# Performance work log

Measured on AMD Instinct MI355X. Metric: run time of the kernel, lower is better.

Reference implementation:

```python
import jax, jax.numpy as jnp
import numpy as np

TGT, BSZ, E, H, HD, P = 256, 64, 1024, 16, 64, 16
TAU = 3.0  # gumbel temperature
SCALE = 1.0 / np.sqrt(HD)


def setup_inputs() -> dict:
    rng = jax.random.key(0)
    ks = jax.random.split(rng, 14)
    n = lambda i, s: jax.random.normal(ks[i], s, dtype=jnp.float32)
    u = jax.random.uniform(ks[7], (BSZ, 2), dtype=jnp.float32, minval=1e-6, maxval=1.0 - 1e-6)
    return {
        'idx': 0,
        'query': n(0, (TGT, BSZ, E)),
        'key': n(1, (TGT, BSZ, E)),
        'value': n(2, (TGT, BSZ, E)),
        'prefix': n(3, (BSZ, 2, P, E)) * 0.5,  # gathered prefix_pool[prompt_ids]
        'batch_weight': jax.random.uniform(ks[4], (BSZ,), dtype=jnp.float32),
        'ori_image_features': n(5, (BSZ, 512)),
        'gumbel_noise': -jnp.log(-jnp.log(u)),  # standard gumbel(0,1) noise
        'in_proj_w': n(8, (3 * E, E)) * 0.02,
        'in_proj_b': jnp.zeros((3 * E,), jnp.float32),
        'out_w': n(9, (E, E)) * 0.02,
        'out_b': jnp.zeros((E,), jnp.float32),
        'gumbel_w': n(10, (2, 512)) * 0.05,
        'gumbel_b': jnp.zeros((2,), jnp.float32),
    }


def _sdpa(q, k, v):
    # q:[b,h,t,d] k,v:[b,h,s,d]
    s = jnp.einsum('bhtd,bhsd->bhts', q, k) * SCALE
    a = jax.nn.softmax(s, axis=-1)
    return jnp.einsum('bhts,bhsd->bhtd', a, v)


def reference(idx, query, key, value, prefix, batch_weight, ori_image_features,
              gumbel_noise, in_proj_w, in_proj_b, out_w, out_b, gumbel_w, gumbel_b):
    tgt, bsz, e = query.shape
    src = key.shape[0]
    # packed in-projection (w chunked into q/k/v blocks)
    w_q, w_k, w_v = jnp.split(in_proj_w, 3, axis=0)
    b_q, b_k, b_v = jnp.split(in_proj_b, 3, axis=0)
    q = query @ w_q.T + b_q            # [t,b,E]
    k = key @ w_k.T + b_k              # [s,b,E]
    v = value @ w_v.T + b_v
    # -> [b,h,t,d]
    q = q.reshape(tgt, bsz, H, HD).transpose(1, 2, 0, 3)
    k = k.reshape(src, bsz, H, HD).transpose(1, 2, 0, 3)
    v = v.reshape(src, bsz, H, HD).transpose(1, 2, 0, 3)
    # prefix k/v: [b,P,E] -> [b,h,P,d] (no in-projection, used raw as in source)
    pk = prefix[:, 0].reshape(bsz, P, H, HD).transpose(0, 2, 1, 3)
    pv = prefix[:, 1].reshape(bsz, P, H, HD).transpose(0, 2, 1, 3)

    attn = _sdpa(q, k, v)                      # [b,h,t,d]
    attn_flat = attn.transpose(2, 0, 1, 3).reshape(tgt * bsz, e)  # (t,b) row order

    attn_pre = _sdpa(q, pk, pv) * batch_weight[:, None, None, None]
    attn_pre_flat = attn_pre.transpose(2, 0, 1, 3).reshape(tgt * bsz, e)

    # gumbel-softmax gate (soft), one 2-way gate per sample
    logits = ori_image_features @ gumbel_w.T + gumbel_b           # [b,2]
    gumbel = jax.nn.softmax((logits + gumbel_noise) / TAU, axis=-1)
    gate = jnp.repeat(gumbel, tgt, axis=0)                        # [b*t,2] (b,t) order, as in source
    combined = attn_flat * gate[:, :1] + (attn_flat + attn_pre_flat) * gate[:, 1:2]

    out = combined @ out_w.T + out_b
    return out.reshape(tgt, bsz, e)
```

## Files before the change

kernel.cpp:

```cpp
#include <hip/hip_runtime.h>

typedef __attribute__((ext_vector_type(8))) short bf16x8;
typedef __attribute__((ext_vector_type(4))) float f32x4;
typedef __attribute__((ext_vector_type(8))) unsigned short ushort8;
typedef __attribute__((ext_vector_type(4))) unsigned short ushort4v;
typedef __attribute__((ext_vector_type(4))) float float4v;
typedef __attribute__((ext_vector_type(2))) unsigned int uint2v;
typedef __attribute__((ext_vector_type(4))) unsigned int uint4v;

#define TGT 256
#define BSZ 64
#define EMB 1024
#define NH 16
#define HD 64
#define PP 16

__device__ __forceinline__ float b2f(unsigned short u) {
  return __builtin_bit_cast(float, ((unsigned int)u) << 16);
}
__device__ __forceinline__ unsigned short f2b(float f) {
  unsigned int u = __builtin_bit_cast(unsigned int, f);
  u += 0x7fffu + ((u >> 16) & 1u);
  return (unsigned short)(u >> 16);
}
__device__ __forceinline__ unsigned int pack2(float lo, float hi) {
  return (unsigned int)f2b(lo) | ((unsigned int)f2b(hi) << 16);
}
__device__ __forceinline__ f32x4 mfma16(bf16x8 a, bf16x8 b, f32x4 c) {
  return __builtin_amdgcn_mfma_f32_16x16x32_bf16(a, b, c, 0, 0, 0);
}
__device__ __forceinline__ void gl_lds16(const unsigned short* g, unsigned short* l) {
  __builtin_amdgcn_global_load_lds(
      (const __attribute__((address_space(1))) unsigned int*)g,
      (__attribute__((address_space(3))) unsigned int*)l, 16, 0, 0);
}

__global__ __launch_bounds__(64) void gate_kernel(
    const float* __restrict__ feat, const float* __restrict__ gw,
    const float* __restrict__ gb, const float* __restrict__ noise,
    float* __restrict__ g1) {
  const int b = blockIdx.x, lane = threadIdx.x;
  float a0 = 0.f, a1 = 0.f;
  for (int i = lane; i < 512; i += 64) {
    float f = feat[b * 512 + i];
    a0 += f * gw[i];
    a1 += f * gw[512 + i];
  }
#pragma unroll
  for (int off = 32; off >= 1; off >>= 1) {
    a0 += __shfl_xor(a0, off);
    a1 += __shfl_xor(a1, off);
  }
  if (lane == 0) {
    float l0 = (a0 + gb[0] + noise[b * 2 + 0]) * (1.0f / 3.0f);
    float l1 = (a1 + gb[1] + noise[b * 2 + 1]) * (1.0f / 3.0f);
    float mm = fmaxf(l0, l1);
    float e0 = __expf(l0 - mm), e1 = __expf(l1 - mm);
    g1[b] = e1 / (e0 + e1);
  }
}

__global__ __launch_bounds__(256) void cast_bf16_kernel(
    const float* __restrict__ in, unsigned short* __restrict__ out, int n8) {
  int i = blockIdx.x * blockDim.x + threadIdx.x;
  const int stride = gridDim.x * blockDim.x;
  for (; i < n8; i += stride) {
    const float4v* p = (const float4v*)(in + (size_t)i * 8);
    float4v v0 = p[0], v1 = p[1];
    ushort8 o = {f2b(v0[0]), f2b(v0[1]), f2b(v0[2]), f2b(v0[3]),
                 f2b(v1[0]), f2b(v1[1]), f2b(v1[2]), f2b(v1[3])};
    *(ushort8*)(out + (size_t)i * 8) = o;
  }
}

#define A128_ISSUE(t)                                    \
  {                                                      \
    const float* _p = a32p + (size_t)(t) * 32;           \
    ar[(t) & 1][0] = *(const float4v*)_p;                \
    ar[(t) & 1][1] = *(const float4v*)(_p + 4);          \
  }
#define A128_WRITE(t)                                                   \
  {                                                                     \
    float4v* v = ar[(t) & 1];                                           \
    uint4v h = {pack2(v[0][0], v[0][1]), pack2(v[0][2], v[0][3]),       \
                pack2(v[1][0], v[1][1]), pack2(v[1][2], v[1][3])};      \
    *(uint4v*)&As[(t) & 1][swA] = h;                                    \
  }
#define B128_STAGE(s)                                    \
  {                                                      \
    int k0s = (s) * 32;                                  \
    unsigned short* d = &Bs[(s) & 3][wl];                \
    gl_lds16(b0p + k0s, d);                              \
    gl_lds16(b1p + k0s, d + 4096);                       \
  }
#define G128_STEP(s, DO_IA, DO_SB, DO_W)                              \
  {                                                                   \
    const unsigned short* Ab = &As[(s) & 1][0];                       \
    const unsigned short* Bb = &Bs[(s) & 3][0];                       \
    bf16x8 af[4], bfr[4];                                             \
    _Pragma("unroll") for (int mi = 0; mi < 4; ++mi)                  \
        af[mi] = *(const bf16x8*)&Ab[aoff + mi * 512];                \
    _Pragma("unroll") for (int ni = 0; ni < 2; ++ni)                  \
        bfr[ni] = *(const bf16x8*)&Bb[boff + ni * 512];               \
    if (DO_IA) A128_ISSUE((s) + 2);                                   \
    __builtin_amdgcn_s_barrier();                                     \
    __builtin_amdgcn_s_setprio(1);                                    \
    _Pragma("unroll") for (int mi = 0; mi < 4; ++mi) {                \
      acc[mi][0] = mfma16(af[mi], bfr[0], acc[mi][0]);                \
      acc[mi][1] = mfma16(af[mi], bfr[1], acc[mi][1]);                \
    }                                                                 \
    __builtin_amdgcn_s_setprio(0);                                    \
    __builtin_amdgcn_s_barrier();                                     \
    _Pragma("unroll") for (int ni = 2; ni < 4; ++ni)                  \
        bfr[ni] = *(const bf16x8*)&Bb[boff + ni * 512];               \
    if (DO_SB) B128_STAGE((s) + 3);                                   \
    __builtin_amdgcn_s_barrier();                                     \
    __builtin_amdgcn_s_setprio(1);                                    \
    _Pragma("unroll") for (int mi = 0; mi < 4; ++mi) {                \
      acc[mi][2] = mfma16(af[mi], bfr[2], acc[mi][2]);                \
      acc[mi][3] = mfma16(af[mi], bfr[3], acc[mi][3]);                \
    }                                                                 \
    __builtin_amdgcn_s_setprio(0);                                    \
    if (DO_W) A128_WRITE((s) + 1);                                    \
  }
#define STEP_WAIT(cntstr)                                \
  asm volatile("s_waitcnt " cntstr ::: "memory");        \
  __builtin_amdgcn_sched_barrier(0);                     \
  __builtin_amdgcn_s_barrier();

template <int QSCALE>
__global__ __launch_bounds__(512, 4) void gemm128f_kernel(
    const float* __restrict__ A, const unsigned short* __restrict__ W,
    const float* __restrict__ bias, unsigned short* __restrict__ Cv) {
  constexpr int K = 1024, N = 1024;
  __shared__ __attribute__((aligned(16))) unsigned short As[2][4096];
  __shared__ __attribute__((aligned(16))) unsigned short Bs[4][8192];
  const int tid = threadIdx.x;
  const int wv = tid >> 6, lane = tid & 63;
  const int l15 = lane & 15, kg = lane >> 4;
  const int bid = blockIdx.x;
  const int cpx = gridDim.x >> 3;
  const int wg = (bid & 7) * cpx + (bid >> 3);
  const int m0 = (wg >> 2) * 128, n0 = (wg & 3) * 256;
  const int wmL = (wv >> 2) * 64, wnL = (wv & 3) * 64;

  const int sr = wv * 16 + (lane >> 2);
  const int sc = ((lane & 3) * 8) ^ (((sr >> 1) & 3) << 3);
  const unsigned short* b0p = W + (size_t)(n0 + sr) * K + sc;
  const unsigned short* b1p = b0p + (size_t)128 * K;
  const int wl = wv * 512;

  const int arr = tid >> 2;
  const float* a32p = A + (size_t)(m0 + arr) * K + (tid & 3) * 8;
  const int swA = arr * 32 + (((tid & 3) ^ ((arr >> 1) & 3)) << 3);
  float4v ar[2][2];

  const int x = ((l15 >> 1) & 3) << 3;
  const int aoff = (wmL + l15) * 32 + ((kg * 8) ^ x);
  const int boff = (wnL + l15) * 32 + ((kg * 8) ^ x);

  f32x4 acc[4][4];
#pragma unroll
  for (int i = 0; i < 4; ++i)
#pragma unroll
    for (int j = 0; j < 4; ++j) acc[i][j] = (f32x4){0.f, 0.f, 0.f, 0.f};

  A128_ISSUE(0); B128_STAGE(0); A128_ISSUE(1); B128_STAGE(1); B128_STAGE(2);
  A128_WRITE(0);
  STEP_WAIT("vmcnt(6) lgkmcnt(0)")

#pragma unroll
  for (int s = 0; s < 30; ++s) {
    G128_STEP(s, (s < 30), (s < 29), 1);
    STEP_WAIT("vmcnt(6) lgkmcnt(0)")
  }
  G128_STEP(30, 0, 0, 1);
  STEP_WAIT("vmcnt(0) lgkmcnt(0)")
  G128_STEP(31, 0, 0, 0);

#pragma unroll
  for (int mi = 0; mi < 4; ++mi) {
#pragma unroll
    for (int ni = 0; ni < 4; ++ni) {
      int col = n0 + wnL + ni * 16 + l15;
      float bcol = bias[col];
#pragma unroll
      for (int r = 0; r < 4; ++r) {
        int row = m0 + wmL + mi * 16 + kg * 4 + r;
        float v = acc[mi][ni][r] + bcol;
        if constexpr (QSCALE) v *= 0.125f;
        int t = row >> 6, bb = row & 63, hh = col >> 6, dd = col & 63;
        Cv[(size_t)((bb * 16 + hh) * 256 + t) * 64 + dd] = f2b(v);
      }
    }
  }
}

#define AOFF(s) (((s) >> 1) * 16384 + ((s)&1) * 32)
#define STAGE_A(s)                                       \
  {                                                      \
    const unsigned short* _ap = abf + AOFF(s);           \
    unsigned short* d = &As[(s) & 3][wl];                \
    gl_lds16(_ap, d);                                    \
    gl_lds16(_ap + 128, d + 4096);                       \
  }
#define STAGE_B(s)                                       \
  {                                                      \
    int k0s = (s) * 32;                                  \
    unsigned short* d = &Bs[(s) & 3][wl];                \
    gl_lds16(b0p + k0s, d);                              \
    gl_lds16(b1p + k0s, d + 4096);                       \
  }
#define GEMM_STEP(s, DO_STAGE)                                        \
  {                                                                   \
    const unsigned short* Ab = &As[(s) & 3][0];                       \
    const unsigned short* Bb = &Bs[(s) & 3][0];                       \
    bf16x8 af[8], bfr[4];                                             \
    _Pragma("unroll") for (int mi = 0; mi < 8; ++mi)                  \
        af[mi] = *(const bf16x8*)&Ab[aoff + mi * 512];                \
    _Pragma("unroll") for (int ni = 0; ni < 2; ++ni)                  \
        bfr[ni] = *(const bf16x8*)&Bb[boff + ni * 512];               \
    if (DO_STAGE) STAGE_A((s) + 3);                                   \
    __builtin_amdgcn_s_barrier();                                     \
    __builtin_amdgcn_s_setprio(1);                                    \
    _Pragma("unroll") for (int mi = 0; mi < 8; ++mi) {                \
      acc[mi][0] = mfma16(af[mi], bfr[0], acc[mi][0]);                \
      acc[mi][1] = mfma16(af[mi], bfr[1], acc[mi][1]);                \
    }                                                                 \
    __builtin_amdgcn_s_setprio(0);                                    \
    __builtin_amdgcn_s_barrier();                                     \
    _Pragma("unroll") for (int ni = 2; ni < 4; ++ni)                  \
        bfr[ni] = *(const bf16x8*)&Bb[boff + ni * 512];               \
    if (DO_STAGE) STAGE_B((s) + 3);                                   \
    __builtin_amdgcn_s_barrier();                                     \
    __builtin_amdgcn_s_setprio(1);                                    \
    _Pragma("unroll") for (int mi = 0; mi < 8; ++mi) {                \
      acc[mi][2] = mfma16(af[mi], bfr[2], acc[mi][2]);                \
      acc[mi][3] = mfma16(af[mi], bfr[3], acc[mi][3]);                \
    }                                                                 \
    __builtin_amdgcn_s_setprio(0);                                    \
  }

__global__ __launch_bounds__(512, 2) void gemm256_kernel(
    const unsigned short* __restrict__ A, const unsigned short* __restrict__ W,
    const float* __restrict__ bias, float* __restrict__ Cv) {
  constexpr int K = 1024, N = 1024;
  __shared__ __attribute__((aligned(16))) unsigned short As[4][8192];
  __shared__ __attribute__((aligned(16))) unsigned short Bs[4][8192];
  const int tid = threadIdx.x;
  const int wv = tid >> 6, lane = tid & 63;
  const int l15 = lane & 15, kg = lane >> 4;
  const int bid = blockIdx.x;
  const int cpx = gridDim.x >> 3;
  const int wg = (bid & 7) * cpx + (bid >> 3);
  const int m0 = (wg >> 2) * 256, n0 = (wg & 3) * 256;
  const int wmL = (wv >> 2) * 128, wnL = (wv & 3) * 64;

  const int sr = wv * 16 + (lane >> 2);
  const int sc = ((lane & 3) * 8) ^ (((sr >> 1) & 3) << 3);
  const int srg = m0 + sr;
  const unsigned short* abf =
      A + (size_t)(srg & 63) * 262144 + (srg >> 6) * 64 + sc;
  const unsigned short* b0p = W + (size_t)(n0 + sr) * K + sc;
  const unsigned short* b1p = b0p + (size_t)128 * K;
  const int wl = wv * 512;

  const int x = ((l15 >> 1) & 3) << 3;
  const int aoff = (wmL + l15) * 32 + ((kg * 8) ^ x);
  const int boff = (wnL + l15) * 32 + ((kg * 8) ^ x);

  f32x4 acc[8][4];
#pragma unroll
  for (int i = 0; i < 8; ++i)
#pragma unroll
    for (int j = 0; j < 4; ++j) acc[i][j] = (f32x4){0.f, 0.f, 0.f, 0.f};

  STAGE_A(0); STAGE_B(0); STAGE_A(1); STAGE_B(1); STAGE_A(2); STAGE_B(2);
  STEP_WAIT("vmcnt(8)")

  for (int s = 0; s < 29; ++s) {
    GEMM_STEP(s, 1);
    STEP_WAIT("vmcnt(8)")
  }
  GEMM_STEP(29, 0);
  STEP_WAIT("vmcnt(4)")
  GEMM_STEP(30, 0);
  STEP_WAIT("vmcnt(0)")
  GEMM_STEP(31, 0);

#pragma unroll
  for (int mi = 0; mi < 8; ++mi) {
#pragma unroll
    for (int ni = 0; ni < 4; ++ni) {
      int col = n0 + wnL + ni * 16 + l15;
      float bcol = bias[col];
#pragma unroll
      for (int r = 0; r < 4; ++r) {
        int row = m0 + wmL + mi * 16 + kg * 4 + r;
        Cv[(size_t)row * N + col] = acc[mi][ni][r] + bcol;
      }
    }
  }
}

__global__ __launch_bounds__(512) void attn_kernel(
    const unsigned short* __restrict__ qb, const unsigned short* __restrict__ kb,
    const unsigned short* __restrict__ vb, const float* __restrict__ prefix,
    const float* __restrict__ bw, const float* __restrict__ g1,
    unsigned short* __restrict__ comb) {
  const int b = blockIdx.x, h = blockIdx.y;
  __shared__ __attribute__((aligned(16))) unsigned short Kl[256][64];
  __shared__ __attribute__((aligned(16))) unsigned short Vt[64 * 256];
  __shared__ __attribute__((aligned(16))) unsigned short PKl[16][64];
  __shared__ __attribute__((aligned(16))) unsigned short PVt[64][32];
  __shared__ __attribute__((aligned(16))) unsigned short Plds[8][16][40];
  unsigned short* Cb = &Kl[0][0];
  const int tid = threadIdx.x;
  const int wv = tid >> 6, lane = tid & 63;
  const size_t slab = (size_t)(b * NH + h) * 16384;

#pragma unroll
  for (int it = 0; it < 4; ++it) {
    int cid = tid + it * 512;
    int j = cid >> 3, c = cid & 7;
    gl_lds16(kb + slab + (size_t)j * 64 + ((c ^ (j & 7)) << 3),
             &Kl[0][0] + (size_t)(it * 512 + wv * 64) * 8);
    ushort8 vv = *(const ushort8*)(vb + slab + (size_t)j * 64 + (c << 3));
#pragma unroll
    for (int i = 0; i < 8; ++i) {
      int gran = (j >> 3) ^ i ^ c;
      Vt[(c * 8 + i) * 256 + gran * 8 + (j & 7)] = vv[i];
    }
  }
  if (tid < 256) {
    int arr = tid >> 7, cid = tid & 127;
    int sp = cid >> 3, c = cid & 7;
    const float* src = prefix + ((size_t)(b * 2 + arr) * PP + sp) * EMB + h * HD + c * 8;
    float4v v0 = *(const float4v*)src;
    float4v v1 = *(const float4v*)(src + 4);
    if (arr == 0) {
      ushort8 o = {f2b(v0[0]), f2b(v0[1]), f2b(v0[2]), f2b(v0[3]),
                   f2b(v1[0]), f2b(v1[1]), f2b(v1[2]), f2b(v1[3])};
      *(ushort8*)&PKl[sp][((c ^ (sp & 7)) << 3)] = o;
    } else {
#pragma unroll
      for (int i = 0; i < 8; ++i)
        PVt[c * 8 + i][sp] = f2b(i < 4 ? v0[i] : v1[i - 4]);
    }
  } else if (tid < 384) {
    int cid = tid - 256;
    *(ushort8*)&PVt[cid >> 1][16 + (cid & 1) * 8] = (ushort8){0, 0, 0, 0, 0, 0, 0, 0};
  }
  __syncthreads();

  const int l15 = lane & 15, g = lane >> 4;
  const int swl = l15 & 7;
  const float bwb = bw[b];
  unsigned short(&Pw)[16][40] = Plds[wv];

  const int t0 = wv * 32 + l15;
  const size_t qbase = slab + (size_t)t0 * 64;
  bf16x8 qf[2][2];
  qf[0][0] = *(const bf16x8*)(qb + qbase + g * 8);
  qf[0][1] = *(const bf16x8*)(qb + qbase + 32 + g * 8);
  qf[1][0] = *(const bf16x8*)(qb + qbase + 1024 + g * 8);
  qf[1][1] = *(const bf16x8*)(qb + qbase + 1024 + 32 + g * 8);

  f32x4 O[2][4];
#pragma unroll
  for (int st = 0; st < 2; ++st)
#pragma unroll
    for (int dt = 0; dt < 4; ++dt) O[st][dt] = (f32x4){0.f, 0.f, 0.f, 0.f};
  float m[2] = {-3.0e38f, -3.0e38f}, l[2] = {0.f, 0.f};

#pragma unroll
  for (int ch = 0; ch < 8; ++ch) {
    const int rA = ch * 32 + l15, rB = rA + 16;
    bf16x8 ka0 = *(const bf16x8*)&Kl[rA][((g ^ swl) << 3)];
    bf16x8 ka1 = *(const bf16x8*)&Kl[rA][(((4 + g) ^ swl) << 3)];
    bf16x8 kb0 = *(const bf16x8*)&Kl[rB][((g ^ swl) << 3)];
    bf16x8 kb1 = *(const bf16x8*)&Kl[rB][(((4 + g) ^ swl) << 3)];
    f32x4 s[2][2];
#pragma unroll
    for (int st = 0; st < 2; ++st) {
      s[st][0] = (f32x4){0.f, 0.f, 0.f, 0.f};
      s[st][1] = (f32x4){0.f, 0.f, 0.f, 0.f};
      s[st][0] = mfma16(ka0, qf[st][0], s[st][0]);
      s[st][0] = mfma16(ka1, qf[st][1], s[st][0]);
      s[st][1] = mfma16(kb0, qf[st][0], s[st][1]);
      s[st][1] = mfma16(kb1, qf[st][1], s[st][1]);
    }
    bf16x8 pf[2];
#pragma unroll
    for (int st = 0; st < 2; ++st) {
      f32x4 sa = s[st][0], sb = s[st][1];
      float mx = fmaxf(fmaxf(fmaxf(sa[0], sa[1]), fmaxf(sa[2], sa[3])),
                       fmaxf(fmaxf(sb[0], sb[1]), fmaxf(sb[2], sb[3])));
      mx = fmaxf(mx, __shfl_xor(mx, 16));
      mx = fmaxf(mx, __shfl_xor(mx, 32));
      if (__ballot(mx > m[st] + 8.0f) != 0ull) {
        float mn = fmaxf(m[st], mx);
        float f = __expf(m[st] - mn);
        m[st] = mn;
        l[st] *= f;
#pragma unroll
        for (int dt = 0; dt < 4; ++dt)
#pragma unroll
          for (int r = 0; r < 4; ++r) O[st][dt][r] *= f;
      }
      float pA[4], pB[4];
#pragma unroll
      for (int r = 0; r < 4; ++r) {
        pA[r] = __expf(sa[r] - m[st]);
        pB[r] = __expf(sb[r] - m[st]);
      }
      uint2v wa = {pack2(pA[0], pA[1]), pack2(pA[2], pA[3])};
      uint2v wb2 = {pack2(pB[0], pB[1]), pack2(pB[2], pB[3])};
      *(uint2v*)&Pw[l15][g * 4] = wa;
      *(uint2v*)&Pw[l15][16 + g * 4] = wb2;
      float sloc = b2f((unsigned short)(wa[0] & 0xffff)) + b2f((unsigned short)(wa[0] >> 16)) +
                   b2f((unsigned short)(wa[1] & 0xffff)) + b2f((unsigned short)(wa[1] >> 16)) +
                   b2f((unsigned short)(wb2[0] & 0xffff)) + b2f((unsigned short)(wb2[0] >> 16)) +
                   b2f((unsigned short)(wb2[1] & 0xffff)) + b2f((unsigned short)(wb2[1] >> 16));
      l[st] += sloc;
      pf[st] = *(const bf16x8*)&Pw[l15][g * 8];
    }
#pragma unroll
    for (int dt = 0; dt < 4; ++dt) {
      const int drow = dt * 16 + l15;
      const int gran = (ch * 4 + g) ^ (drow & 7) ^ (drow >> 3);
      bf16x8 vf = *(const bf16x8*)&Vt[drow * 256 + gran * 8];
      O[0][dt] = mfma16(vf, pf[0], O[0][dt]);
      O[1][dt] = mfma16(vf, pf[1], O[1][dt]);
    }
  }

#pragma unroll
  for (int st = 0; st < 2; ++st) {
    float lf = l[st];
    lf += __shfl_xor(lf, 16);
    lf += __shfl_xor(lf, 32);
    float inv = 1.0f / lf;
#pragma unroll
    for (int dt = 0; dt < 4; ++dt)
#pragma unroll
      for (int r = 0; r < 4; ++r) O[st][dt][r] *= inv;
  }

  {
    bf16x8 pk0 = *(const bf16x8*)&PKl[l15][((g ^ swl) << 3)];
    bf16x8 pk1 = *(const bf16x8*)&PKl[l15][(((4 + g) ^ swl) << 3)];
    bf16x8 ppf[2];
#pragma unroll
    for (int st = 0; st < 2; ++st) {
      f32x4 sp4 = (f32x4){0.f, 0.f, 0.f, 0.f};
      sp4 = mfma16(pk0, qf[st][0], sp4);
      sp4 = mfma16(pk1, qf[st][1], sp4);
      float pm = fmaxf(fmaxf(sp4[0], sp4[1]), fmaxf(sp4[2], sp4[3]));
      pm = fmaxf(pm, __shfl_xor(pm, 16));
      pm = fmaxf(pm, __shfl_xor(pm, 32));
      float pe[4], pl = 0.f;
#pragma unroll
      for (int r = 0; r < 4; ++r) {
        pe[r] = __expf(sp4[r] - pm);
        pl += pe[r];
      }
      pl += __shfl_xor(pl, 16);
      pl += __shfl_xor(pl, 32);
      float cpre = g1[(t0 + 16 * st) >> 2] * bwb / pl;
#pragma unroll
      for (int r = 0; r < 4; ++r) pe[r] *= cpre;
      *(uint2v*)&Pw[l15][g * 4] = (uint2v){pack2(pe[0], pe[1]), pack2(pe[2], pe[3])};
      *(uint2v*)&Pw[l15][16 + g * 4] = (uint2v){0u, 0u};
      ppf[st] = *(const bf16x8*)&Pw[l15][g * 8];
    }
#pragma unroll
    for (int dt = 0; dt < 4; ++dt) {
      bf16x8 pvf = *(const bf16x8*)&PVt[dt * 16 + l15][g * 8];
      O[0][dt] = mfma16(pvf, ppf[0], O[0][dt]);
      O[1][dt] = mfma16(pvf, ppf[1], O[1][dt]);
    }
  }

  __syncthreads();
#pragma unroll
  for (int st = 0; st < 2; ++st) {
    int t = wv * 32 + st * 16 + l15;
#pragma unroll
    for (int dt = 0; dt < 4; ++dt) {
#pragma unroll
      for (int u = 0; u < 2; ++u) {
        unsigned int pw = pack2(O[st][dt][2 * u], O[st][dt][2 * u + 1]);
        int d = dt * 16 + g * 4 + 2 * u;
        *(unsigned int*)&Cb[t * 64 + (((d >> 3) ^ (t & 7)) << 3) + (d & 7)] = pw;
      }
    }
  }
  __syncthreads();
#pragma unroll
  for (int it = 0; it < 4; ++it) {
    int cid = tid + it * 512;
    int j = cid >> 3, c = cid & 7;
    ushort8 row = *(const ushort8*)&Cb[j * 64 + ((c ^ (j & 7)) << 3)];
    *(ushort8*)(comb + slab + (size_t)j * 64 + (c << 3)) = row;
  }
}

extern "C" void kernel_launch(void* const* d_in, const int* in_sizes, int n_in,
                              void* d_out, int out_size, void* d_ws, size_t ws_size,
                              hipStream_t stream) {
  const float* query = (const float*)d_in[1];
  const float* key = (const float*)d_in[2];
  const float* value = (const float*)d_in[3];
  const float* prefix = (const float*)d_in[4];
  const float* bw = (const float*)d_in[5];
  const float* feat = (const float*)d_in[6];
  const float* noise = (const float*)d_in[7];
  const float* ipw = (const float*)d_in[8];
  const float* ipb = (const float*)d_in[9];
  const float* outw = (const float*)d_in[10];
  const float* outb = (const float*)d_in[11];
  const float* gw = (const float*)d_in[12];
  const float* gb = (const float*)d_in[13];
  float* out = (float*)d_out;

  char* ws = (char*)d_ws;
  const size_t MATB = (size_t)16384 * 1024;
  unsigned short* qb = (unsigned short*)ws;
  unsigned short* kb = qb + MATB;
  unsigned short* vb = kb + MATB;
  unsigned short* cb = vb + MATB;
  unsigned short* wip = cb + MATB;
  unsigned short* wo = wip + (size_t)3072 * 1024;
  float* g1 = (float*)(wo + (size_t)1024 * 1024);

  gate_kernel<<<64, 64, 0, stream>>>(feat, gw, gb, noise, g1);

  cast_bf16_kernel<<<1536, 256, 0, stream>>>(ipw, wip, 3072 * 1024 / 8);
  cast_bf16_kernel<<<512, 256, 0, stream>>>(outw, wo, 1024 * 1024 / 8);

  gemm128f_kernel<1><<<512, 512, 0, stream>>>(query, wip, ipb, qb);
  gemm128f_kernel<0><<<512, 512, 0, stream>>>(key, wip + (size_t)1024 * 1024, ipb + 1024, kb);
  gemm128f_kernel<0><<<512, 512, 0, stream>>>(value, wip + (size_t)2048 * 1024, ipb + 2048, vb);

  attn_kernel<<<dim3(64, 16), 512, 0, stream>>>(qb, kb, vb, prefix, bw, g1, cb);

  gemm256_kernel<<<256, 512, 0, stream>>>(cb, wo, outb, out);
}
```

Baseline: 274.2 us.

## Merge Q/K/V projections into one 256x256-tile kernel and simplify GEMM step barriers

Replaces the three separate 128x256-tile fp32-input projection launches with a single proj3 kernel using a 3-wide grid y dimension and 256x256 tiles. The A operand is converted from fp32 into double-buffered LDS, with each thread loading two rows. Both the projection and output GEMM steps now load all B fragments up front and issue all 32 MFMAs without intra-step barriers. The aim is fewer launches, more reuse per tile and less barrier overhead, at the cost of higher register pressure and lower occupancy (2 blocks per CU).

```diff
diff --git a/kernel.cpp b/kernel.cpp
--- a/kernel.cpp
+++ b/kernel.cpp
@@ -73,113 +73,124 @@
   }
 }
 
-#define A128_ISSUE(t)                                    \
-  {                                                      \
-    const float* _p = a32p + (size_t)(t) * 32;           \
-    ar[(t) & 1][0] = *(const float4v*)_p;                \
-    ar[(t) & 1][1] = *(const float4v*)(_p + 4);          \
-  }
-#define A128_WRITE(t)                                                   \
-  {                                                                     \
-    float4v* v = ar[(t) & 1];                                           \
-    uint4v h = {pack2(v[0][0], v[0][1]), pack2(v[0][2], v[0][3]),       \
-                pack2(v[1][0], v[1][1]), pack2(v[1][2], v[1][3])};      \
-    *(uint4v*)&As[(t) & 1][swA] = h;                                    \
-  }
-#define B128_STAGE(s)                                    \
-  {                                                      \
-    int k0s = (s) * 32;                                  \
-    unsigned short* d = &Bs[(s) & 3][wl];                \
-    gl_lds16(b0p + k0s, d);                              \
-    gl_lds16(b1p + k0s, d + 4096);                       \
-  }
-#define G128_STEP(s, DO_IA, DO_SB, DO_W)                              \
-  {                                                                   \
-    const unsigned short* Ab = &As[(s) & 1][0];                       \
-    const unsigned short* Bb = &Bs[(s) & 3][0];                       \
-    bf16x8 af[4], bfr[4];                                             \
-    _Pragma("unroll") for (int mi = 0; mi < 4; ++mi)                  \
-        af[mi] = *(const bf16x8*)&Ab[aoff + mi * 512];                \
-    _Pragma("unroll") for (int ni = 0; ni < 2; ++ni)                  \
-        bfr[ni] = *(const bf16x8*)&Bb[boff + ni * 512];               \
-    if (DO_IA) A128_ISSUE((s) + 2);                                   \
-    __builtin_amdgcn_s_barrier();                                     \
-    __builtin_amdgcn_s_setprio(1);                                    \
-    _Pragma("unroll") for (int mi = 0; mi < 4; ++mi) {                \
-      acc[mi][0] = mfma16(af[mi], bfr[0], acc[mi][0]);                \
-      acc[mi][1] = mfma16(af[mi], bfr[1], acc[mi][1]);                \
-    }                                                                 \
-    __builtin_amdgcn_s_setprio(0);                                    \
-    __builtin_amdgcn_s_barrier();                                     \
-    _Pragma("unroll") for (int ni = 2; ni < 4; ++ni)                  \
-        bfr[ni] = *(const bf16x8*)&Bb[boff + ni * 512];               \
-    if (DO_SB) B128_STAGE((s) + 3);                                   \
-    __builtin_amdgcn_s_barrier();                                     \
-    __builtin_amdgcn_s_setprio(1);                                    \
-    _Pragma("unroll") for (int mi = 0; mi < 4; ++mi) {                \
-      acc[mi][2] = mfma16(af[mi], bfr[2], acc[mi][2]);                \
-      acc[mi][3] = mfma16(af[mi], bfr[3], acc[mi][3]);                \
-    }                                                                 \
-    __builtin_amdgcn_s_setprio(0);                                    \
-    if (DO_W) A128_WRITE((s) + 1);                                    \
-  }
 #define STEP_WAIT(cntstr)                                \
   asm volatile("s_waitcnt " cntstr ::: "memory");        \
   __builtin_amdgcn_sched_barrier(0);                     \
   __builtin_amdgcn_s_barrier();
 
-template <int QSCALE>
-__global__ __launch_bounds__(512, 4) void gemm128f_kernel(
-    const float* __restrict__ A, const unsigned short* __restrict__ W,
-    const float* __restrict__ bias, unsigned short* __restrict__ Cv) {
-  constexpr int K = 1024, N = 1024;
-  __shared__ __attribute__((aligned(16))) unsigned short As[2][4096];
+#define P3_ISSUE(t, P)                                   \
+  {                                                      \
+    const float* _p = a32p + (size_t)(t) * 32;           \
+    ar[P][0] = *(const float4v*)_p;                      \
+    ar[P][1] = *(const float4v*)(_p + 4);                \
+    ar[P][2] = *(const float4v*)(_p + 131072);           \
+    ar[P][3] = *(const float4v*)(_p + 131072 + 4);       \
+  }
+#define P3_WRITE(P)                                                     \
+  {                                                                     \
+    float4v* v = ar[P];                                                 \
+    uint4v h0 = {pack2(v[0][0], v[0][1]), pack2(v[0][2], v[0][3]),      \
+                 pack2(v[1][0], v[1][1]), pack2(v[1][2], v[1][3])};     \
+    uint4v h1 = {pack2(v[2][0], v[2][1]), pack2(v[2][2], v[2][3]),      \
+                 pack2(v[3][0], v[3][1]), pack2(v[3][2], v[3][3])};     \
+    unsigned short* d = &As[P][swA];                                    \
+    *(uint4v*)d = h0;                                                   \
+    *(uint4v*)(d + 4096) = h1;                                          \
+  }
+#define B_STAGE_SLOT(s, SL)                              \
+  {                                                      \
+    int k0s = (s) * 32;                                  \
+    unsigned short* d = &Bs[SL][wl];                     \
+    gl_lds16(b0p + k0s, d);                              \
+    gl_lds16(b1p + k0s, d + 4096);                       \
+  }
+#define P3_STEP(s, PAR, BS, DO_IA, DO_SB, DO_W)                       \
+  {                                                                   \
+    const unsigned short* Ab = &As[PAR][0];                           \
+    const unsigned short* Bb = &Bs[BS][0];                            \
+    bf16x8 af[8], bfr[4];                                             \
+    _Pragma("unroll") for (int mi = 0; mi < 8; ++mi)                  \
+        af[mi] = *(const bf16x8*)&Ab[aoff + mi * 512];                \
+    _Pragma("unroll") for (int ni = 0; ni < 4; ++ni)                  \
+        bfr[ni] = *(const bf16x8*)&Bb[boff + ni * 512];               \
+    if (DO_IA) P3_ISSUE((s) + 2, PAR);                                \
+    if (DO_SB) B_STAGE_SLOT((s) + 3, ((BS) + 3) & 3);                 \
+    __builtin_amdgcn_s_setprio(1);                                    \
+    _Pragma("unroll") for (int mi = 0; mi < 8; ++mi)                  \
+      _Pragma("unroll") for (int ni = 0; ni < 4; ++ni)                \
+        acc[mi][ni] = mfma16(af[mi], bfr[ni], acc[mi][ni]);           \
+    __builtin_amdgcn_s_setprio(0);                                    \
+    if (DO_W) P3_WRITE((PAR) ^ 1);                 \
+  }
+
+__global__ __launch_bounds__(512, 2) void proj3_kernel(
+    const float* __restrict__ q, const float* __restrict__ kk,
+    const float* __restrict__ vv, const unsigned short* __restrict__ W3,
+    const float* __restrict__ bias3, unsigned short* __restrict__ C3) {
+  constexpr int K = 1024;
+  __shared__ __attribute__((aligned(16))) unsigned short As[2][8192];
   __shared__ __attribute__((aligned(16))) unsigned short Bs[4][8192];
+  const int pj = blockIdx.y;
+  const float* A = (pj == 0) ? q : ((pj == 1) ? kk : vv);
+  const unsigned short* W = W3 + (size_t)pj * 1024 * 1024;
+  const float* bias = bias3 + pj * 1024;
+  unsigned short* Cv = C3 + (size_t)pj * 16384 * 1024;
+  const float qsc = (pj == 0) ? 0.125f : 1.0f;
+
   const int tid = threadIdx.x;
   const int wv = tid >> 6, lane = tid & 63;
   const int l15 = lane & 15, kg = lane >> 4;
   const int bid = blockIdx.x;
   const int cpx = gridDim.x >> 3;
   const int wg = (bid & 7) * cpx + (bid >> 3);
-  const int m0 = (wg >> 2) * 128, n0 = (wg & 3) * 256;
-  const int wmL = (wv >> 2) * 64, wnL = (wv & 3) * 64;
+  const int m0 = (wg >> 2) * 256, n0 = (wg & 3) * 256;
+  const int wmL = (wv >> 2) * 128, wnL = (wv & 3) * 64;
 
   const int sr = wv * 16 + (lane >> 2);
   const int sc = ((lane & 3) * 8) ^ (((sr >> 1) & 3) << 3);
+  const float* a32p = A + (size_t)(m0 + sr) * K + (lane & 3) * 8;
+  const int swA = sr * 32 + (((lane & 3) ^ ((sr >> 1) & 3)) << 3);
+  float4v ar[2][4];
   const unsigned short* b0p = W + (size_t)(n0 + sr) * K + sc;
   const unsigned short* b1p = b0p + (size_t)128 * K;
   const int wl = wv * 512;
 
-  const int arr = tid >> 2;
-  const float* a32p = A + (size_t)(m0 + arr) * K + (tid & 3) * 8;
-  const int swA = arr * 32 + (((tid & 3) ^ ((arr >> 1) & 3)) << 3);
-  float4v ar[2][2];
-
   const int x = ((l15 >> 1) & 3) << 3;
   const int aoff = (wmL + l15) * 32 + ((kg * 8) ^ x);
   const int boff = (wnL + l15) * 32 + ((kg * 8) ^ x);
 
-  f32x4 acc[4][4];
-#pragma unroll
-  for (int i = 0; i < 4; ++i)
+  f32x4 acc[8][4];
+#pragma unroll
+  for (int i = 0; i < 8; ++i)
 #pragma unroll
     for (int j = 0; j < 4; ++j) acc[i][j] = (f32x4){0.f, 0.f, 0.f, 0.f};
 
-  A128_ISSUE(0); B128_STAGE(0); A128_ISSUE(1); B128_STAGE(1); B128_STAGE(2);
-  A128_WRITE(0);
-  STEP_WAIT("vmcnt(6) lgkmcnt(0)")
-
-#pragma unroll
-  for (int s = 0; s < 30; ++s) {
-    G128_STEP(s, (s < 30), (s < 29), 1);
-    STEP_WAIT("vmcnt(6) lgkmcnt(0)")
-  }
-  G128_STEP(30, 0, 0, 1);
+  P3_ISSUE(0, 0); B_STAGE_SLOT(0, 0); P3_ISSUE(1, 1); B_STAGE_SLOT(1, 1);
+  B_STAGE_SLOT(2, 2);
+  P3_WRITE(0);
+  STEP_WAIT("vmcnt(8) lgkmcnt(0)")
+
+#pragma unroll 1
+  for (int sb = 0; sb < 28; sb += 4) {
+    P3_STEP(sb + 0, 0, 0, 1, 1, 1);
+    STEP_WAIT("vmcnt(8) lgkmcnt(0)")
+    P3_STEP(sb + 1, 1, 1, 1, 1, 1);
+    STEP_WAIT("vmcnt(8) lgkmcnt(0)")
+    P3_STEP(sb + 2, 0, 2, 1, 1, 1);
+    STEP_WAIT("vmcnt(8) lgkmcnt(0)")
+    P3_STEP(sb + 3, 1, 3, 1, 1, 1);
+    STEP_WAIT("vmcnt(8) lgkmcnt(0)")
+  }
+  P3_STEP(28, 0, 0, 1, 1, 1);
+  STEP_WAIT("vmcnt(8) lgkmcnt(0)")
+  P3_STEP(29, 1, 1, 1, 0, 1);
+  STEP_WAIT("vmcnt(8) lgkmcnt(0)")
+  P3_STEP(30, 0, 2, 0, 0, 1);
   STEP_WAIT("vmcnt(0) lgkmcnt(0)")
-  G128_STEP(31, 0, 0, 0);
-
-#pragma unroll
-  for (int mi = 0; mi < 4; ++mi) {
+  P3_STEP(31, 1, 3, 0, 0, 0);
+
+#pragma unroll
+  for (int mi = 0; mi < 8; ++mi) {
 #pragma unroll
     for (int ni = 0; ni < 4; ++ni) {
       int col = n0 + wnL + ni * 16 + l15;
@@ -187,8 +198,7 @@
 #pragma unroll
       for (int r = 0; r < 4; ++r) {
         int row = m0 + wmL + mi * 16 + kg * 4 + r;
-        float v = acc[mi][ni][r] + bcol;
-        if constexpr (QSCALE) v *= 0.125f;
+        float v = (acc[mi][ni][r] + bcol) * qsc;
         int t = row >> 6, bb = row & 63, hh = col >> 6, dd = col & 63;
         Cv[(size_t)((bb * 16 + hh) * 256 + t) * 64 + dd] = f2b(v);
       }
@@ -196,52 +206,42 @@
   }
 }
 
-#define AOFF(s) (((s) >> 1) * 16384 + ((s)&1) * 32)
-#define STAGE_A(s)                                       \
+#define O_AOFF(s) (((s) >> 1) * 16384 + ((s)&1) * 32)
+#define O_STAGE_A(s)                                     \
   {                                                      \
-    const unsigned short* _ap = abf + AOFF(s);           \
+    const unsigned short* _ap = abf + O_AOFF(s);         \
     unsigned short* d = &As[(s) & 3][wl];                \
     gl_lds16(_ap, d);                                    \
     gl_lds16(_ap + 128, d + 4096);                       \
   }
-#define STAGE_B(s)                                       \
+#define O_STAGE_B(s)                                     \
   {                                                      \
     int k0s = (s) * 32;                                  \
     unsigned short* d = &Bs[(s) & 3][wl];                \
     gl_lds16(b0p + k0s, d);                              \
     gl_lds16(b1p + k0s, d + 4096);                       \
   }
-#define GEMM_STEP(s, DO_STAGE)                                        \
+#define O_STEP(s, DO_STAGE)                                           \
   {                                                                   \
     const unsigned short* Ab = &As[(s) & 3][0];                       \
     const unsigned short* Bb = &Bs[(s) & 3][0];                       \
     bf16x8 af[8], bfr[4];                                             \
     _Pragma("unroll") for (int mi = 0; mi < 8; ++mi)                  \
         af[mi] = *(const bf16x8*)&Ab[aoff + mi * 512];                \
-    _Pragma("unroll") for (int ni = 0; ni < 2; ++ni)                  \
+    _Pragma("unroll") for (int ni = 0; ni < 4; ++ni)                  \
         bfr[ni] = *(const bf16x8*)&Bb[boff + ni * 512];               \
-    if (DO_STAGE) STAGE_A((s) + 3);                                   \
-    __builtin_amdgcn_s_barrier();                                     \
+    if (DO_STAGE) {                                                   \
+      O_STAGE_A((s) + 3);                                             \
+      O_STAGE_B((s) + 3);                                             \
+    }                                                                 \
     __builtin_amdgcn_s_setprio(1);                                    \
-    _Pragma("unroll") for (int mi = 0; mi < 8; ++mi) {                \
-      acc[mi][0] = mfma16(af[mi], bfr[0], acc[mi][0]);                \
-      acc[mi][1] = mfma16(af[mi], bfr[1], acc[mi][1]);                \
-    }                                                                 \
+    _Pragma("unroll") for (int mi = 0; mi < 8; ++mi)                  \
+      _Pragma("unroll") for (int ni = 0; ni < 4; ++ni)                \
+        acc[mi][ni] = mfma16(af[mi], bfr[ni], acc[mi][ni]);           \
     __builtin_amdgcn_s_setprio(0);                                    \
-    __builtin_amdgcn_s_barrier();                                     \
-    _Pragma("unroll") for (int ni = 2; ni < 4; ++ni)                  \
-        bfr[ni] = *(const bf16x8*)&Bb[boff + ni * 512];               \
-    if (DO_STAGE) STAGE_B((s) + 3);                                   \
-    __builtin_amdgcn_s_barrier();                                     \
-    __builtin_amdgcn_s_setprio(1);                                    \
-    _Pragma("unroll") for (int mi = 0; mi < 8; ++mi) {                \
-      acc[mi][2] = mfma16(af[mi], bfr[2], acc[mi][2]);                \
-      acc[mi][3] = mfma16(af[mi], bfr[3], acc[mi][3]);                \
-    }                                                                 \
-    __builtin_amdgcn_s_setprio(0);                                    \
-  }
-
-__global__ __launch_bounds__(512, 2) void gemm256_kernel(
+  }
+
+__global__ __launch_bounds__(512, 2) void gemm256o_kernel(
     const unsigned short* __restrict__ A, const unsigned short* __restrict__ W,
     const float* __restrict__ bias, float* __restrict__ Cv) {
   constexpr int K = 1024, N = 1024;
@@ -275,18 +275,18 @@
 #pragma unroll
     for (int j = 0; j < 4; ++j) acc[i][j] = (f32x4){0.f, 0.f, 0.f, 0.f};
 
-  STAGE_A(0); STAGE_B(0); STAGE_A(1); STAGE_B(1); STAGE_A(2); STAGE_B(2);
+  O_STAGE_A(0); O_STAGE_B(0); O_STAGE_A(1); O_STAGE_B(1); O_STAGE_A(2); O_STAGE_B(2);
   STEP_WAIT("vmcnt(8)")
 
   for (int s = 0; s < 29; ++s) {
-    GEMM_STEP(s, 1);
+    O_STEP(s, 1);
     STEP_WAIT("vmcnt(8)")
   }
-  GEMM_STEP(29, 0);
+  O_STEP(29, 0);
   STEP_WAIT("vmcnt(4)")
-  GEMM_STEP(30, 0);
+  O_STEP(30, 0);
   STEP_WAIT("vmcnt(0)")
-  GEMM_STEP(31, 0);
+  O_STEP(31, 0);
 
 #pragma unroll
   for (int mi = 0; mi < 8; ++mi) {
@@ -539,11 +539,9 @@
   cast_bf16_kernel<<<1536, 256, 0, stream>>>(ipw, wip, 3072 * 1024 / 8);
   cast_bf16_kernel<<<512, 256, 0, stream>>>(outw, wo, 1024 * 1024 / 8);
 
-  gemm128f_kernel<1><<<512, 512, 0, stream>>>(query, wip, ipb, qb);
-  gemm128f_kernel<0><<<512, 512, 0, stream>>>(key, wip + (size_t)1024 * 1024, ipb + 1024, kb);
-  gemm128f_kernel<0><<<512, 512, 0, stream>>>(value, wip + (size_t)2048 * 1024, ipb + 2048, vb);
+  proj3_kernel<<<dim3(256, 3), 512, 0, stream>>>(query, key, value, wip, ipb, qb);
 
   attn_kernel<<<dim3(64, 16), 512, 0, stream>>>(qb, kb, vb, prefix, bw, g1, cb);
 
-  gemm256_kernel<<<256, 512, 0, stream>>>(cb, wo, outb, out);
-}
+  gemm256o_kernel<<<256, 512, 0, stream>>>(cb, wo, outb, out);
+}
```

After: 264.2 us. 3.7% less time.
